# Optimization experiments

Hardware: AMD Instinct MI355X
Metric: run time of the kernel (lower is better)

Reference implementation:

```python
import jax, jax.numpy as jnp
import numpy as np

NUM_SKILLS = 300
EMB_SIZE = 256
CURVE_DIM = 64  # splits: 21 / 21 / 22
B, S = 512, 200


def setup_inputs() -> dict:
    key = jax.random.key(0)
    ks = jax.random.split(key, 11)
    d3 = CURVE_DIM // 3
    dm = d3 + CURVE_DIM % 3
    return {
        "q": jax.random.randint(ks[0], (B, S), 0, NUM_SKILLS, dtype=jnp.int32),
        "r": jax.random.randint(ks[1], (B, S), 0, 2, dtype=jnp.int32),
        "qry": jax.random.randint(ks[2], (B, S), 0, NUM_SKILLS, dtype=jnp.int32),
        "skill_w": jax.random.normal(ks[3], (d3,), jnp.float32),
        "skill_b": jax.random.normal(ks[4], (d3,), jnp.float32),
        "att_w": jax.random.normal(ks[5], (d3,), jnp.float32),
        "att_b": jax.random.normal(ks[6], (d3,), jnp.float32),
        "mast_w": jax.random.normal(ks[7], (dm,), jnp.float32),
        "mast_b": jax.random.normal(ks[8], (dm,), jnp.float32),
        "proj_w": jax.random.normal(ks[9], (EMB_SIZE, CURVE_DIM), jnp.float32) * 0.05,
        "proj_b": jax.random.normal(ks[10], (EMB_SIZE,), jnp.float32),
    }


def _running_counts(q, r):
    """Per-(b,t) running attempt count and correct count for the skill at (b,t).
    Returns attempts[B,S], correct[B,S] (float32), valid[B,S] (bool)."""
    b, s = q.shape
    rows = jnp.arange(b)
    valid = (q >= 0) & (q < NUM_SKILLS)
    idx = jnp.clip(q, 0, NUM_SKILLS - 1)

    def step(carry, xs):
        att, cor = carry  # [B, NUM_SKILLS] int32
        it, rt, vt = xs   # [B] each
        att = att.at[rows, it].add(vt.astype(jnp.int32))
        cor = cor.at[rows, it].add((rt * vt).astype(jnp.int32))
        return (att, cor), (att[rows, it], cor[rows, it])

    init = (jnp.zeros((b, NUM_SKILLS), jnp.int32), jnp.zeros((b, NUM_SKILLS), jnp.int32))
    xs = (idx.T, r.T, valid.T)  # scan over time
    _, (a_t, c_t) = jax.lax.scan(step, init, xs)
    return a_t.T.astype(jnp.float32), c_t.T.astype(jnp.float32), valid


def reference(q, r, qry, skill_w, skill_b, att_w, att_b, mast_w, mast_b, proj_w, proj_b):
    attempts, correct, valid = _running_counts(q, r)  # [B,S]
    mastery = correct / jnp.maximum(attempts, 1.0)
    skill_f = q.astype(jnp.float32)
    # Linear(1, d): scalar * w + b, broadcast over [B,S]
    s_enc = skill_f[..., None] * skill_w + skill_b        # [B,S,21]
    n_enc = attempts[..., None] * att_w + att_b           # [B,S,21]
    m_enc = mastery[..., None] * mast_w + mast_b          # [B,S,22]
    tup = jnp.concatenate([s_enc, n_enc, m_enc], axis=-1)  # [B,S,CURVE_DIM]
    traj = jnp.einsum('bsc,ec->bse', tup, proj_w) + proj_b  # [B,S,EMB]
    return jnp.where(valid[..., None], traj, 0.0)
```

## Files before the change

### kernel.cpp

```cpp
#include <hip/hip_runtime.h>

constexpr int NUM_SKILLS = 300;
constexpr int EMB = 256;
constexpr int CD  = 64;
constexpr int D3  = 21;
constexpr int DM  = 22;
constexpr int SEQ = 200;

typedef float vf4 __attribute__((ext_vector_type(4)));

__global__ __launch_bounds__(256)
void traj_enc_kernel(const int* __restrict__ q, const int* __restrict__ r,
                     const float* __restrict__ skill_w, const float* __restrict__ skill_b,
                     const float* __restrict__ att_w,   const float* __restrict__ att_b,
                     const float* __restrict__ mast_w,  const float* __restrict__ mast_b,
                     const float* __restrict__ proj_w,  const float* __restrict__ proj_b,
                     float* __restrict__ out)
{
    __shared__ __align__(16) float sA[EMB];
    __shared__ __align__(16) float sB[EMB];
    __shared__ __align__(16) float sC[EMB];
    __shared__ __align__(16) float sD[EMB];
    __shared__ float s_skill[SEQ], s_att[SEQ], s_mast[SEQ], s_valid[SEQ];
    __shared__ int   s_q[SEQ], s_r[SEQ];

    const int tid = threadIdx.x;
    const int b   = blockIdx.x;

    if (tid < SEQ) {
        s_q[tid] = q[b * SEQ + tid];
        s_r[tid] = r[b * SEQ + tid];
    }

    {
        const float* pw = proj_w + tid * CD;
        float ca = 0.f, cb = 0.f, cc = 0.f, cd = 0.f;
        #pragma unroll
        for (int i = 0; i < D3; ++i) { float w = pw[i];        ca = fmaf(w, skill_w[i], ca); cd = fmaf(w, skill_b[i], cd); }
        #pragma unroll
        for (int i = 0; i < D3; ++i) { float w = pw[D3 + i];   cb = fmaf(w, att_w[i],  cb);  cd = fmaf(w, att_b[i],  cd); }
        #pragma unroll
        for (int i = 0; i < DM; ++i) { float w = pw[2*D3 + i]; cc = fmaf(w, mast_w[i], cc);  cd = fmaf(w, mast_b[i], cd); }
        sA[tid] = ca; sB[tid] = cb; sC[tid] = cc; sD[tid] = cd + proj_b[tid];
    }
    __syncthreads();

    if (tid < SEQ) {
        const int myq = s_q[tid];
        const bool v  = (myq >= 0) && (myq < NUM_SKILLS);
        int cnt = 0, cor = 0;
        for (int t = 0; t <= tid; ++t) {
            const int qt = s_q[t];
            const bool m = (qt == myq) && v;
            cnt += m ? 1 : 0;
            cor += m ? s_r[t] : 0;
        }
        const float att = (float)cnt;
        s_skill[tid] = (float)myq;
        s_att[tid]   = att;
        s_mast[tid]  = (float)cor / fmaxf(att, 1.0f);
        s_valid[tid] = v ? 1.0f : 0.0f;
    }
    __syncthreads();

    const int e4   = tid & 63;
    const int ssub = tid >> 6;
    const float4 A4 = *reinterpret_cast<const float4*>(&sA[e4 * 4]);
    const float4 B4 = *reinterpret_cast<const float4*>(&sB[e4 * 4]);
    const float4 C4 = *reinterpret_cast<const float4*>(&sC[e4 * 4]);
    const float4 D4 = *reinterpret_cast<const float4*>(&sD[e4 * 4]);

    vf4* __restrict__ out4 = reinterpret_cast<vf4*>(out) + (size_t)b * SEQ * (EMB / 4);
    #pragma unroll 2
    for (int s0 = 0; s0 < SEQ; s0 += 4) {
        const int s = s0 + ssub;
        const float sk = s_skill[s];
        const float at = s_att[s];
        const float ma = s_mast[s];
        const float v  = s_valid[s];
        vf4 o;
        o.x = v * fmaf(sk, A4.x, fmaf(at, B4.x, fmaf(ma, C4.x, D4.x)));
        o.y = v * fmaf(sk, A4.y, fmaf(at, B4.y, fmaf(ma, C4.y, D4.y)));
        o.z = v * fmaf(sk, A4.z, fmaf(at, B4.z, fmaf(ma, C4.z, D4.z)));
        o.w = v * fmaf(sk, A4.w, fmaf(at, B4.w, fmaf(ma, C4.w, D4.w)));
        __builtin_nontemporal_store(o, &out4[(size_t)s * (EMB / 4) + e4]);
    }
}

extern "C" void kernel_launch(void* const* d_in, const int* in_sizes, int n_in,
                              void* d_out, int out_size, void* d_ws, size_t ws_size,
                              hipStream_t stream)
{
    const int* q        = (const int*)d_in[0];
    const int* r        = (const int*)d_in[1];
    const float* skill_w = (const float*)d_in[3];
    const float* skill_b = (const float*)d_in[4];
    const float* att_w   = (const float*)d_in[5];
    const float* att_b   = (const float*)d_in[6];
    const float* mast_w  = (const float*)d_in[7];
    const float* mast_b  = (const float*)d_in[8];
    const float* proj_w  = (const float*)d_in[9];
    const float* proj_b  = (const float*)d_in[10];
    float* out = (float*)d_out;

    const int B = in_sizes[0] / SEQ;
    traj_enc_kernel<<<B, 256, 0, stream>>>(q, r, skill_w, skill_b, att_w, att_b,
                                           mast_w, mast_b, proj_w, proj_b, out);
}
```

Baseline: 31.49 us.

## Split each sequence across four blocks and vectorize projection weight loads

Launches four blocks per batch row, each computing running counts and writing output for a quarter of the sequence (50 rows), which raises the grid to 2048 blocks to improve occupancy and spread the store traffic. Each block still loads the full q/r row and recomputes the folded projection coefficients, so that setup work is repeated four times. The projection weights are now read as float4 vectors into registers, which raises register pressure.

Result: no change. 31.11 us (-1.2%).

```diff
diff --git a/kernel.cpp b/kernel.cpp
--- a/kernel.cpp
+++ b/kernel.cpp
@@ -6,6 +6,8 @@
 constexpr int D3  = 21;
 constexpr int DM  = 22;
 constexpr int SEQ = 200;
+constexpr int QUARTERS = 4;
+constexpr int ROWS_PB  = SEQ / QUARTERS;
 
 typedef float vf4 __attribute__((ext_vector_type(4)));
 
@@ -21,11 +23,12 @@
     __shared__ __align__(16) float sB[EMB];
     __shared__ __align__(16) float sC[EMB];
     __shared__ __align__(16) float sD[EMB];
-    __shared__ float s_skill[SEQ], s_att[SEQ], s_mast[SEQ], s_valid[SEQ];
+    __shared__ float s_sk[ROWS_PB], s_at[ROWS_PB], s_ma[ROWS_PB], s_va[ROWS_PB];
     __shared__ int   s_q[SEQ], s_r[SEQ];
 
-    const int tid = threadIdx.x;
-    const int b   = blockIdx.x;
+    const int tid  = threadIdx.x;
+    const int b    = blockIdx.x >> 2;
+    const int qs   = (blockIdx.x & 3) * ROWS_PB;
 
     if (tid < SEQ) {
         s_q[tid] = q[b * SEQ + tid];
@@ -33,33 +36,37 @@
     }
 
     {
-        const float* pw = proj_w + tid * CD;
+        const vf4* pw4 = reinterpret_cast<const vf4*>(proj_w + tid * CD);
+        vf4 W[16];
+        #pragma unroll
+        for (int i = 0; i < 16; ++i) W[i] = pw4[i];
+
         float ca = 0.f, cb = 0.f, cc = 0.f, cd = 0.f;
         #pragma unroll
-        for (int i = 0; i < D3; ++i) { float w = pw[i];        ca = fmaf(w, skill_w[i], ca); cd = fmaf(w, skill_b[i], cd); }
+        for (int i = 0; i < D3; ++i) { float w = W[i >> 2][i & 3];              ca = fmaf(w, skill_w[i], ca); cd = fmaf(w, skill_b[i], cd); }
         #pragma unroll
-        for (int i = 0; i < D3; ++i) { float w = pw[D3 + i];   cb = fmaf(w, att_w[i],  cb);  cd = fmaf(w, att_b[i],  cd); }
+        for (int i = 0; i < D3; ++i) { float w = W[(D3 + i) >> 2][(D3 + i) & 3]; cb = fmaf(w, att_w[i],  cb);  cd = fmaf(w, att_b[i],  cd); }
         #pragma unroll
-        for (int i = 0; i < DM; ++i) { float w = pw[2*D3 + i]; cc = fmaf(w, mast_w[i], cc);  cd = fmaf(w, mast_b[i], cd); }
+        for (int i = 0; i < DM; ++i) { float w = W[(2*D3 + i) >> 2][(2*D3 + i) & 3]; cc = fmaf(w, mast_w[i], cc); cd = fmaf(w, mast_b[i], cd); }
         sA[tid] = ca; sB[tid] = cb; sC[tid] = cc; sD[tid] = cd + proj_b[tid];
     }
     __syncthreads();
 
-    if (tid < SEQ) {
-        const int myq = s_q[tid];
+    if (tid < ROWS_PB) {
+        const int row = qs + tid;
+        const int myq = s_q[row];
         const bool v  = (myq >= 0) && (myq < NUM_SKILLS);
         int cnt = 0, cor = 0;
-        for (int t = 0; t <= tid; ++t) {
-            const int qt = s_q[t];
-            const bool m = (qt == myq) && v;
+        for (int t = 0; t <= row; ++t) {
+            const bool m = (s_q[t] == myq) && v;
             cnt += m ? 1 : 0;
             cor += m ? s_r[t] : 0;
         }
         const float att = (float)cnt;
-        s_skill[tid] = (float)myq;
-        s_att[tid]   = att;
-        s_mast[tid]  = (float)cor / fmaxf(att, 1.0f);
-        s_valid[tid] = v ? 1.0f : 0.0f;
+        s_sk[tid] = (float)myq;
+        s_at[tid] = att;
+        s_ma[tid] = (float)cor / fmaxf(att, 1.0f);
+        s_va[tid] = v ? 1.0f : 0.0f;
     }
     __syncthreads();
 
@@ -70,14 +77,23 @@
     const float4 C4 = *reinterpret_cast<const float4*>(&sC[e4 * 4]);
     const float4 D4 = *reinterpret_cast<const float4*>(&sD[e4 * 4]);
 
-    vf4* __restrict__ out4 = reinterpret_cast<vf4*>(out) + (size_t)b * SEQ * (EMB / 4);
-    #pragma unroll 2
-    for (int s0 = 0; s0 < SEQ; s0 += 4) {
+    vf4* __restrict__ out4 = reinterpret_cast<vf4*>(out)
+                           + (size_t)(b * SEQ + qs) * (EMB / 4);
+
+    #pragma unroll 3
+    for (int s0 = 0; s0 + 4 <= ROWS_PB; s0 += 4) {
         const int s = s0 + ssub;
-        const float sk = s_skill[s];
-        const float at = s_att[s];
-        const float ma = s_mast[s];
-        const float v  = s_valid[s];
+        const float sk = s_sk[s], at = s_at[s], ma = s_ma[s], v = s_va[s];
+        vf4 o;
+        o.x = v * fmaf(sk, A4.x, fmaf(at, B4.x, fmaf(ma, C4.x, D4.x)));
+        o.y = v * fmaf(sk, A4.y, fmaf(at, B4.y, fmaf(ma, C4.y, D4.y)));
+        o.z = v * fmaf(sk, A4.z, fmaf(at, B4.z, fmaf(ma, C4.z, D4.z)));
+        o.w = v * fmaf(sk, A4.w, fmaf(at, B4.w, fmaf(ma, C4.w, D4.w)));
+        __builtin_nontemporal_store(o, &out4[(size_t)s * (EMB / 4) + e4]);
+    }
+    if (ssub < 2) {
+        const int s = 48 + ssub;
+        const float sk = s_sk[s], at = s_at[s], ma = s_ma[s], v = s_va[s];
         vf4 o;
         o.x = v * fmaf(sk, A4.x, fmaf(at, B4.x, fmaf(ma, C4.x, D4.x)));
         o.y = v * fmaf(sk, A4.y, fmaf(at, B4.y, fmaf(ma, C4.y, D4.y)));
@@ -104,6 +120,7 @@
     float* out = (float*)d_out;
 
     const int B = in_sizes[0] / SEQ;
-    traj_enc_kernel<<<B, 256, 0, stream>>>(q, r, skill_w, skill_b, att_w, att_b,
-                                           mast_w, mast_b, proj_w, proj_b, out);
+    traj_enc_kernel<<<B * QUARTERS, 256, 0, stream>>>(q, r, skill_w, skill_b,
+                                                      att_w, att_b, mast_w, mast_b,
+                                                      proj_w, proj_b, out);
 }
```
